# Kernel optimization log

Hardware: AMD Instinct MI355X
Metric: run time of the kernel (lower is better)

The kernel has to match this reference:

```python
import jax, jax.numpy as jnp
import numpy as np

OUT = 7          # output_size
SR = 2           # sampling_ratio
SCALE = 1.0 / 16.0  # 1 / feature_stride


def _context_boxes(boxes):
    """8 surrounding cells of a 3x3 grid around each RoI; offset-major concat ([8N,4])."""
    x1, y1, x2, y2 = boxes[:, 0], boxes[:, 1], boxes[:, 2], boxes[:, 3]
    w = (x2 - x1) / 3.0
    h = (y2 - y1) / 3.0
    offs = []
    for i in range(3):
        for j in range(3):
            if i == 1 and j == 1:
                continue
            dx = j * w
            dy = i * h
            offs.append(jnp.stack([x1 + dx, y1 + dy, x1 + dx + w, y1 + dy + h], axis=1))
    return jnp.concatenate(offs, axis=0)


def _roi_align_v2(feat, boxes, scale, out, sr):
    """ROIAlignV2 (aligned=True). feat [C,H,W], boxes [B,4] xyxy -> [B,C,out,out]."""
    C, H, W = feat.shape
    # aligned: half-pixel offset, no max(roi_size, 1)
    x1 = boxes[:, 0] * scale - 0.5
    y1 = boxes[:, 1] * scale - 0.5
    bw = (boxes[:, 2] * scale - 0.5 - x1) / out   # bin width
    bh = (boxes[:, 3] * scale - 0.5 - y1) / out   # bin height
    # sample positions along each axis: start + (bin + (s+0.5)/sr) * bin_size  -> [B, out*sr]
    g = jnp.arange(out * sr) // sr
    s = jnp.arange(out * sr) % sr
    t = g + (s + 0.5) / sr                         # [out*sr]
    ys = y1[:, None] + t[None, :] * bh[:, None]    # [B,S]
    xs = x1[:, None] + t[None, :] * bw[:, None]    # [B,S]

    def axis(p, size):
        valid = (p >= -1.0) & (p <= size)
        p = jnp.clip(p, 0.0, size - 1.0)
        lo = jnp.clip(jnp.floor(p), 0.0, size - 2.0).astype(jnp.int32)
        return lo, p - lo, valid

    yl, fy, vy = axis(ys, H)
    xl, fx, vx = axis(xs, W)
    Y = yl[:, :, None]          # [B,S,1]
    X = xl[:, None, :]          # [B,1,S]
    f00 = feat[:, Y, X]         # [C,B,S,S]
    f01 = feat[:, Y, X + 1]
    f10 = feat[:, Y + 1, X]
    f11 = feat[:, Y + 1, X + 1]
    wy = fy[:, :, None]
    wx = fx[:, None, :]
    v = (f00 * (1 - wy) * (1 - wx) + f01 * (1 - wy) * wx
         + f10 * wy * (1 - wx) + f11 * wy * wx)
    v = v * (vy[:, :, None] & vx[:, None, :]).astype(v.dtype)
    # average the sr x sr samples inside each output bin
    B = boxes.shape[0]
    v = v.reshape(C, B, out, sr, out, sr).mean(axis=(3, 5))
    return v.transpose(1, 0, 2, 3)  # [B,C,out,out]


def setup_inputs() -> dict:
    key = jax.random.key(0)
    k1, k2, k3, k4 = jax.random.split(key, 4)
    features = jax.random.normal(k1, (256, 64, 64), dtype=jnp.float32)  # stride-16 map of a 1024px image
    N = 128
    xy = jax.random.uniform(k2, (N, 2), minval=0.0, maxval=800.0)
    wh = jax.random.uniform(k3, (N, 2), minval=32.0, maxval=220.0)
    boxes = jnp.concatenate([xy, xy + wh], axis=1)                      # [N,4] xyxy, image coords
    w_fuse = jax.random.normal(k4, (256, 2048), dtype=jnp.float32) * 0.02  # Conv2d(2048,256,1) weight
    b_fuse = jnp.zeros((256,), dtype=jnp.float32)
    return {"features": features, "boxes": boxes, "w_fuse": w_fuse, "b_fuse": b_fuse}


def reference(features, boxes, w_fuse, b_fuse):
    N = boxes.shape[0]
    cboxes = _context_boxes(boxes)                               # [8N,4] offset-major
    pooled = _roi_align_v2(features, cboxes, SCALE, OUT, SR)     # [8N,256,7,7]
    chunk = pooled.reshape(N, -1, OUT, OUT)                      # faithful to torch .view(N,-1,7,7)
    out = jnp.einsum('nchw,oc->nohw', chunk, w_fuse) + b_fuse[None, :, None, None]
    return jax.nn.relu(out)                                      # [N,256,7,7]
```

## Files before the change

kernel.cpp:

```cpp
#include <hip/hip_runtime.h>
#include <hip/hip_fp16.h>

#define SCALE (1.0f/16.0f)

typedef __attribute__((ext_vector_type(8))) _Float16 f16x8;
typedef __attribute__((ext_vector_type(4))) float f32x4;
typedef __attribute__((ext_vector_type(16))) float f32x16;
typedef __attribute__((ext_vector_type(4))) unsigned int u32x4;
typedef unsigned int u32;

#define PIN16(W) { _Pragma("unroll") \
    for (int s_ = 0; s_ < 16; ++s_) \
        asm volatile("" : "+v"((W)[s_][0]), "+v"((W)[s_][1]), "+v"((W)[s_][2]), "+v"((W)[s_][3])); }

__device__ __forceinline__ void gload16(const void* g, void* l) {
    __builtin_amdgcn_global_load_lds(
        (const __attribute__((address_space(1))) unsigned int*)g,
        (__attribute__((address_space(3))) unsigned int*)l, 16, 0, 0);
}
__device__ __forceinline__ __half2 asH2(u32 v) {
    union { u32 i; __half2 h; } u; u.i = v; return u.h;
}
__device__ __forceinline__ u32 asU32(__half2 h) {
    union { __half2 h; u32 i; } u; u.h = h; return u.i;
}
__device__ __forceinline__ int dupH2(float f) {
    __half h = __float2half_rn(f);
    __half2 d; d.x = h; d.y = h;
    union { __half2 h2; int i; } u; u.h2 = d; return u.i;
}

__global__ void k_prep(const float* __restrict__ feat, __half* __restrict__ featT,
                       const float* __restrict__ wf, __half* __restrict__ wr) {
    __shared__ float t[64][65];
    int b = blockIdx.x;
    if (b < 256) {
        int cb = (b >> 6) << 6;
        int pb = (b & 63) << 6;
        int lx = threadIdx.x & 63, ly = threadIdx.x >> 6;
#pragma unroll
        for (int i = 0; i < 16; ++i) {
            int cl = i*4 + ly;
            t[cl][lx] = feat[(size_t)(cb + cl) * 4096 + pb + lx];
        }
        __syncthreads();
#pragma unroll
        for (int i = 0; i < 16; ++i) {
            int pl = i*4 + ly;
            featT[(size_t)(pb + pl) * 256 + cb + lx] = __float2half_rn(t[lx][pl]);
        }
    } else {
        int ch = (b - 256) * 256 + threadIdx.x;
        int l  = ch & 63;
        int sk = (ch >> 6) & 15;
        int ot = (ch >> 10) & 7;
        int j  = ch >> 13;
        int o = ot*32 + (l & 31);
        int k = j*256 + sk*16 + (l >> 5)*8;
        const float* src = wf + (size_t)o*2048 + k;
        f32x4 a = *(const f32x4*)src;
        f32x4 bb = *(const f32x4*)(src + 4);
        f16x8 p;
#pragma unroll
        for (int u = 0; u < 4; ++u) p[u] = (_Float16)a[u];
#pragma unroll
        for (int u = 0; u < 4; ++u) p[4+u] = (_Float16)bb[u];
        *((f16x8*)wr + ch) = p;
    }
}

__global__ void __launch_bounds__(512) k_fused(
    const __half* __restrict__ featT,
    const float* __restrict__ boxes,
    const __half* __restrict__ wr,
    const float* __restrict__ bfuse,
    float* __restrict__ out)
{
    __shared__ char patch[2][32768];
    __shared__ char Pl[2][16384];
    __shared__ int4 tabs[4][2][7];
    __shared__ int  pbs[4][2];

    int tid = threadIdx.x;
    int lane = tid & 63, wid = tid >> 6;
    int r31 = lane & 31, l5 = lane >> 5;
    int oq = wid & 3, kh = wid >> 2;
    int bid = blockIdx.x;
    int n  = bid & 127;
    int hh = bid >> 7;
    int HWn = hh ? 17 : 32;

    int nb_base = (n & 15) * 8;
    int off = n >> 4;
    int t3 = off + (off >= 4 ? 1 : 0);
    int ci = t3 / 3, cj = t3 - ci*3;

    f32x16 acc0, acc1;
#pragma unroll
    for (int i = 0; i < 16; ++i) { acc0[i] = 0.f; acc1[i] = 0.f; }

    auto tablesW = [&](int jj, int isy, bool active) {
        if (active) {
            int nbx = nb_base + jj;
            float bx1 = boxes[nbx*4+0], by1 = boxes[nbx*4+1];
            float bx2 = boxes[nbx*4+2], by2 = boxes[nbx*4+3];
            float w3 = (bx2-bx1)*(1.f/3.f), h3 = (by2-by1)*(1.f/3.f);
            float org  = isy ? (by1 + ci*h3)*SCALE - 0.5f : (bx1 + cj*w3)*SCALE - 0.5f;
            float step = (isy ? h3 : w3) * (SCALE*(1.f/14.f));
            float sc = isy ? 0.25f : 1.f;
            float p = org + ((float)lane + 0.5f)*step;
            float pc = fminf(fmaxf(p, 0.f), 63.f);
            float fl = fminf(floorf(pc), 62.f);
            float fr = pc - fl;
            float c0 = __shfl(fl, 2*lane);
            float c1 = __shfl(fl, 2*lane+1);
            float f  = __shfl(fr, 2*lane);
            float f2 = __shfl(fr, 2*lane+1);
            float fl0 = __shfl(fl, 0);
            int base = min((int)fl0, 56);
            float d = c1 - c0;
            float a0 = sc*((1.f-f) + (1.f-d)*(1.f-f2));
            float a1 = sc*(f + (1.f-d)*f2 + d*(1.f-f2));
            float a2 = sc*(d*f2);
            if (lane < 7) {
                int4 e;
                e.x = (int)c0 - base;
                e.y = dupH2(a0); e.z = dupH2(a1); e.w = dupH2(a2);
                tabs[jj & 3][isy][lane] = e;
            }
            if (lane == 0) pbs[jj & 3][isy] = base;
        }
    };

    auto patchStage = [&](int jj) {
        int xb = pbs[jj & 3][0], yb = pbs[jj & 3][1];
        const __half* src = featT + ((size_t)((yb + wid)*64 + xb))*256 + lane*8;
        char* dst = patch[jj & 1] + wid*4096;
#pragma unroll
        for (int seg = 0; seg < 4; ++seg)
            gload16(src + seg*512, dst + seg*1024);
    };

    auto pool = [&](int jj) {
        int buf = jj & 1;
        int co = tid & 31;
        int e0 = tid >> 5;
        const char* pb = patch[buf] + co*16;
        for (int e = e0; e < HWn; e += 16) {
            int g = hh*32 + e;
            int h = (g*37) >> 8, w = g - h*7;
            int4 tx = tabs[jj & 3][0][w], ty = tabs[jj & 3][1][h];
            int px0 = tx.x, py0 = ty.x;
            int lx2 = min(px0 + 2, 7), ly2 = min(py0 + 2, 7);
            const char* r0 = pb + (py0*8 + px0)*512;
            const char* r1 = pb + (min(py0+1,7)*8 + px0)*512;
            const char* r2 = pb + (ly2*8 + px0)*512;
            int dx2 = (lx2 - px0)*512;
            u32x4 F00 = *(const u32x4*)(r0);
            u32x4 F01 = *(const u32x4*)(r0 + 512);
            u32x4 F02 = *(const u32x4*)(r0 + dx2);
            u32x4 F10 = *(const u32x4*)(r1);
            u32x4 F11 = *(const u32x4*)(r1 + 512);
            u32x4 F12 = *(const u32x4*)(r1 + dx2);
            u32x4 F20 = *(const u32x4*)(r2);
            u32x4 F21 = *(const u32x4*)(r2 + 512);
            u32x4 F22 = *(const u32x4*)(r2 + dx2);
            __half2 xa = asH2(tx.y), xb2 = asH2(tx.z), xc = asH2(tx.w);
            __half2 ya = asH2(ty.y), yb2 = asH2(ty.z), yc = asH2(ty.w);
            u32x4 res;
#pragma unroll
            for (int s = 0; s < 4; ++s) {
                __half2 q0 = __hfma2(asH2(F02[s]), xc, __hfma2(asH2(F01[s]), xb2, __hmul2(asH2(F00[s]), xa)));
                __half2 q1 = __hfma2(asH2(F12[s]), xc, __hfma2(asH2(F11[s]), xb2, __hmul2(asH2(F10[s]), xa)));
                __half2 q2 = __hfma2(asH2(F22[s]), xc, __hfma2(asH2(F21[s]), xb2, __hmul2(asH2(F20[s]), xa)));
                res[s] = asU32(__hfma2(q2, yc, __hfma2(q1, yb2, __hmul2(q0, ya))));
            }
            *(u32x4*)(Pl[buf] + e*512 + ((co*16) ^ ((e & 7) << 4))) = res;
        }
    };

    u32x4 WfA[16], WfB[16];
    auto prefW = [&](u32x4* dst, int j) {
#pragma unroll
        for (int t = 0; t < 2; ++t) {
            int ot = oq*2 + t;
            const u32x4* wb = (const u32x4*)wr + ((size_t)((j*8 + ot)*16 + kh*8))*64 + lane;
#pragma unroll
            for (int s = 0; s < 8; ++s) dst[t*8 + s] = wb[s*64];
        }
    };

    auto gemm = [&](const u32x4* Wsrc, int j) {
        const char* plb = (j & 1) ? Pl[1] : Pl[0];
        f16x8 pf[8];
#pragma unroll
        for (int s = 0; s < 8; ++s) {
            int sk = kh*8 + s;
            int byo = r31*512 + ((sk*32 + l5*16) ^ ((r31 & 7) << 4));
            pf[s] = *(const f16x8*)(plb + byo);
        }
#pragma unroll
        for (int s = 0; s < 8; ++s) {
            acc0 = __builtin_amdgcn_mfma_f32_32x32x16_f16(
                __builtin_bit_cast(f16x8, Wsrc[s]), pf[s], acc0, 0, 0, 0);
            acc1 = __builtin_amdgcn_mfma_f32_32x32x16_f16(
                __builtin_bit_cast(f16x8, Wsrc[8 + s]), pf[s], acc1, 0, 0, 0);
        }
    };

    tablesW(wid >> 1, wid & 1, wid < 6);
    __syncthreads();
    prefW(WfA, 0);
    patchStage(0);
    patchStage(1);
    PIN16(WfA);
    __syncthreads();
    pool(0);
    __syncthreads();

#pragma unroll
    for (int j = 0; j < 8; ++j) {
        if (j < 7) prefW((j & 1) ? WfA : WfB, j+1);
        if (j < 6) patchStage(j+2);
        gemm((j & 1) ? WfB : WfA, j);
        if (j < 7) pool(j+1);
        if (j < 5) tablesW(j+3, wid, wid < 2);
        if (j < 7) { if (j & 1) { PIN16(WfA); } else { PIN16(WfB); } }
        __syncthreads();
    }

    float* red = (float*)&patch[0][0];
    if (kh == 1) {
#pragma unroll
        for (int t = 0; t < 2; ++t) {
            f32x16 a = t ? acc1 : acc0;
#pragma unroll
            for (int q = 0; q < 4; ++q) {
                f32x4 v;
#pragma unroll
                for (int i = 0; i < 4; ++i) v[i] = a[q*4 + i];
                int byo = (oq*2 + t)*4096 + r31*128 + ((q*32 + l5*16) ^ ((r31 & 7) << 4));
                *(f32x4*)((char*)red + byo) = v;
            }
        }
    }
    __syncthreads();
    if (kh == 0) {
        int hw = hh*32 + r31;
        bool ok = hw < 49;
        float* ob = out + (size_t)n*12544 + hw;
#pragma unroll
        for (int t = 0; t < 2; ++t) {
            f32x16 a = t ? acc1 : acc0;
            int otb = (oq*2 + t)*32;
#pragma unroll
            for (int q = 0; q < 4; ++q) {
                int byo = (oq*2 + t)*4096 + r31*128 + ((q*32 + l5*16) ^ ((r31 & 7) << 4));
                f32x4 r = *(const f32x4*)((const char*)red + byo);
#pragma unroll
                for (int i = 0; i < 4; ++i) {
                    int o = otb + q*8 + l5*4 + i;
                    float v = a[q*4 + i] + r[i] + bfuse[o];
                    if (ok) ob[(size_t)o*49] = fmaxf(v, 0.f);
                }
            }
        }
    }
}

extern "C" void kernel_launch(void* const* d_in, const int* in_sizes, int n_in,
                              void* d_out, int out_size, void* d_ws, size_t ws_size,
                              hipStream_t stream) {
    const float* feat  = (const float*)d_in[0];
    const float* boxes = (const float*)d_in[1];
    const float* wf    = (const float*)d_in[2];
    const float* bfuse = (const float*)d_in[3];
    float* out = (float*)d_out;

    char* ws = (char*)d_ws;
    __half* wr    = (__half*)ws;
    __half* featT = (__half*)(ws + (1u<<20));

    k_prep<<<512, 256, 0, stream>>>(feat, featT, wf, wr);
    k_fused<<<256, 512, 0, stream>>>(featT, boxes, wr, bfuse, out);
}
```

Before: 31.00 us.

## Split fused RoI-pool GEMM across output-channel halves with smaller blocks

The grid goes from 256 blocks of 512 threads to 512 blocks of 256 threads. Each block now handles half the output channels and a balanced 25/24 spatial split, and the patch buffer changes from double- to single-buffered with a 7-row patch. The goal is more parallelism and balanced work, plus two blocks per CU. In exchange, every block recomputes the pooled features for both channel halves, which duplicates the pooling work. It also adds an extra barrier per iteration and zero-pads the unused GEMM rows.

```diff
diff --git a/kernel.cpp b/kernel.cpp
--- a/kernel.cpp
+++ b/kernel.cpp
@@ -69,14 +69,14 @@
     }
 }
 
-__global__ void __launch_bounds__(512) k_fused(
+__global__ void __launch_bounds__(256, 2) k_fused(
     const __half* __restrict__ featT,
     const float* __restrict__ boxes,
     const __half* __restrict__ wr,
     const float* __restrict__ bfuse,
     float* __restrict__ out)
 {
-    __shared__ char patch[2][32768];
+    __shared__ char patch[28672];
     __shared__ char Pl[2][16384];
     __shared__ int4 tabs[4][2][7];
     __shared__ int  pbs[4][2];
@@ -84,11 +84,13 @@
     int tid = threadIdx.x;
     int lane = tid & 63, wid = tid >> 6;
     int r31 = lane & 31, l5 = lane >> 5;
-    int oq = wid & 3, kh = wid >> 2;
+    int oq = wid & 1, kh = wid >> 1;
     int bid = blockIdx.x;
     int n  = bid & 127;
-    int hh = bid >> 7;
-    int HWn = hh ? 17 : 32;
+    int hh = (bid >> 7) & 1;
+    int oh = bid >> 8;
+    int hw0 = hh * 25;
+    int HWn = hh ? 24 : 25;
 
     int nb_base = (n & 15) * 8;
     int off = n >> 4;
@@ -98,6 +100,16 @@
     f32x16 acc0, acc1;
 #pragma unroll
     for (int i = 0; i < 16; ++i) { acc0[i] = 0.f; acc1[i] = 0.f; }
+
+    {
+        int padrows = 32 - HWn;
+        for (int i = tid; i < padrows*32*2; i += 256) {
+            int b = i / (padrows*32);
+            int rem = i - b*(padrows*32);
+            int row = HWn + (rem >> 5), slot = rem & 31;
+            *(u32x4*)(Pl[b] + row*512 + slot*16) = (u32x4){0,0,0,0};
+        }
+    }
 
     auto tablesW = [&](int jj, int isy, bool active) {
         if (active) {
@@ -132,28 +144,30 @@
         }
     };
 
-    auto patchStage = [&](int jj) {
+    auto stage = [&](int jj) {
         int xb = pbs[jj & 3][0], yb = pbs[jj & 3][1];
-        const __half* src = featT + ((size_t)((yb + wid)*64 + xb))*256 + lane*8;
-        char* dst = patch[jj & 1] + wid*4096;
-#pragma unroll
-        for (int seg = 0; seg < 4; ++seg)
-            gload16(src + seg*512, dst + seg*1024);
+#pragma unroll
+        for (int i = 0; i < 7; ++i) {
+            int seg = wid + 4*i;
+            int row = seg >> 2, q = seg & 3;
+            const __half* src = featT + ((size_t)((yb + row)*64 + xb))*256 + q*512 + lane*8;
+            gload16(src, patch + row*4096 + q*1024);
+        }
     };
 
     auto pool = [&](int jj) {
         int buf = jj & 1;
         int co = tid & 31;
         int e0 = tid >> 5;
-        const char* pb = patch[buf] + co*16;
-        for (int e = e0; e < HWn; e += 16) {
-            int g = hh*32 + e;
+        const char* pb = patch + co*16;
+        for (int e = e0; e < HWn; e += 8) {
+            int g = hw0 + e;
             int h = (g*37) >> 8, w = g - h*7;
             int4 tx = tabs[jj & 3][0][w], ty = tabs[jj & 3][1][h];
             int px0 = tx.x, py0 = ty.x;
-            int lx2 = min(px0 + 2, 7), ly2 = min(py0 + 2, 7);
+            int lx2 = min(px0 + 2, 7), ly2 = min(py0 + 2, 6);
             const char* r0 = pb + (py0*8 + px0)*512;
-            const char* r1 = pb + (min(py0+1,7)*8 + px0)*512;
+            const char* r1 = pb + (min(py0+1,6)*8 + px0)*512;
             const char* r2 = pb + (ly2*8 + px0)*512;
             int dx2 = (lx2 - px0)*512;
             u32x4 F00 = *(const u32x4*)(r0);
@@ -175,7 +189,7 @@
                 __half2 q2 = __hfma2(asH2(F22[s]), xc, __hfma2(asH2(F21[s]), xb2, __hmul2(asH2(F20[s]), xa)));
                 res[s] = asU32(__hfma2(q2, yc, __hfma2(q1, yb2, __hmul2(q0, ya))));
             }
-            *(u32x4*)(Pl[buf] + e*512 + ((co*16) ^ ((e & 7) << 4))) = res;
+            *(u32x4*)(Pl[buf] + e*512 + ((co*16) ^ ((e & 31) << 4))) = res;
         }
     };
 
@@ -183,8 +197,8 @@
     auto prefW = [&](u32x4* dst, int j) {
 #pragma unroll
         for (int t = 0; t < 2; ++t) {
-            int ot = oq*2 + t;
-            const u32x4* wb = (const u32x4*)wr + ((size_t)((j*8 + ot)*16 + kh*8))*64 + lane;
+            int otg = oh*4 + oq*2 + t;
+            const u32x4* wb = (const u32x4*)wr + ((size_t)((j*8 + otg)*16 + kh*8))*64 + lane;
 #pragma unroll
             for (int s = 0; s < 8; ++s) dst[t*8 + s] = wb[s*64];
         }
@@ -196,7 +210,7 @@
 #pragma unroll
         for (int s = 0; s < 8; ++s) {
             int sk = kh*8 + s;
-            int byo = r31*512 + ((sk*32 + l5*16) ^ ((r31 & 7) << 4));
+            int byo = r31*512 + ((sk*32 + l5*16) ^ (r31 << 4));
             pf[s] = *(const f16x8*)(plb + byo);
         }
 #pragma unroll
@@ -208,11 +222,10 @@
         }
     };
 
-    tablesW(wid >> 1, wid & 1, wid < 6);
+    tablesW(wid >> 1, wid & 1, wid < 4);
     __syncthreads();
+    stage(0);
     prefW(WfA, 0);
-    patchStage(0);
-    patchStage(1);
     PIN16(WfA);
     __syncthreads();
     pool(0);
@@ -220,47 +233,48 @@
 
 #pragma unroll
     for (int j = 0; j < 8; ++j) {
-        if (j < 7) prefW((j & 1) ? WfA : WfB, j+1);
-        if (j < 6) patchStage(j+2);
         gemm((j & 1) ? WfB : WfA, j);
+        if (j < 7) {
+            stage(j+1);
+            prefW((j & 1) ? WfA : WfB, j+1);
+            if (j & 1) { PIN16(WfA); } else { PIN16(WfB); }
+        }
+        __syncthreads();
         if (j < 7) pool(j+1);
-        if (j < 5) tablesW(j+3, wid, wid < 2);
-        if (j < 7) { if (j & 1) { PIN16(WfA); } else { PIN16(WfB); } }
+        if (j < 6) tablesW(j+2, wid, wid < 2);
         __syncthreads();
     }
 
-    float* red = (float*)&patch[0][0];
+    float* red = (float*)patch;
     if (kh == 1) {
 #pragma unroll
         for (int t = 0; t < 2; ++t) {
             f32x16 a = t ? acc1 : acc0;
 #pragma unroll
-            for (int q = 0; q < 4; ++q) {
+            for (int q4 = 0; q4 < 4; ++q4) {
                 f32x4 v;
 #pragma unroll
-                for (int i = 0; i < 4; ++i) v[i] = a[q*4 + i];
-                int byo = (oq*2 + t)*4096 + r31*128 + ((q*32 + l5*16) ^ ((r31 & 7) << 4));
-                *(f32x4*)((char*)red + byo) = v;
+                for (int i = 0; i < 4; ++i) v[i] = a[q4*4 + i];
+                *(f32x4*)((char*)red + (oq*2 + t)*4096 + r31*128 + q4*32 + l5*16) = v;
             }
         }
     }
     __syncthreads();
     if (kh == 0) {
-        int hw = hh*32 + r31;
-        bool ok = hw < 49;
+        int hw = hw0 + r31;
+        bool ok = r31 < HWn;
         float* ob = out + (size_t)n*12544 + hw;
 #pragma unroll
         for (int t = 0; t < 2; ++t) {
             f32x16 a = t ? acc1 : acc0;
-            int otb = (oq*2 + t)*32;
-#pragma unroll
-            for (int q = 0; q < 4; ++q) {
-                int byo = (oq*2 + t)*4096 + r31*128 + ((q*32 + l5*16) ^ ((r31 & 7) << 4));
-                f32x4 r = *(const f32x4*)((const char*)red + byo);
+            int otb = oh*128 + (oq*2 + t)*32;
+#pragma unroll
+            for (int q4 = 0; q4 < 4; ++q4) {
+                f32x4 r = *(const f32x4*)((const char*)red + (oq*2 + t)*4096 + r31*128 + q4*32 + l5*16);
 #pragma unroll
                 for (int i = 0; i < 4; ++i) {
-                    int o = otb + q*8 + l5*4 + i;
-                    float v = a[q*4 + i] + r[i] + bfuse[o];
+                    int o = otb + q4*8 + l5*4 + i;
+                    float v = a[q4*4 + i] + r[i] + bfuse[o];
                     if (ok) ob[(size_t)o*49] = fmaxf(v, 0.f);
                 }
             }
@@ -282,5 +296,5 @@
     __half* featT = (__half*)(ws + (1u<<20));
 
     k_prep<<<512, 256, 0, stream>>>(feat, featT, wf, wr);
-    k_fused<<<256, 512, 0, stream>>>(featT, boxes, wr, bfuse, out);
-}
+    k_fused<<<512, 256, 0, stream>>>(featT, boxes, wr, bfuse, out);
+}
```

Measured after the change: 36.63 us. 18.2% more time.
